# Kernel tuning notes

Measured on AMD Instinct MI355X. Metric: run time of the kernel, lower is better.

Reference implementation:

```python
import jax, jax.numpy as jnp
import numpy as np

D_MODEL = 512
D_FFN = 4 * D_MODEL
EPS = 1e-5


def layer_norm(x, gamma, beta):
    mu = jnp.mean(x, axis=-1, keepdims=True)
    var = jnp.mean(jnp.square(x - mu), axis=-1, keepdims=True)
    return (x - mu) * jax.lax.rsqrt(var + EPS) * gamma + beta


def setup_inputs() -> dict:
    key = jax.random.key(0)
    ks = jax.random.split(key, 12)
    B, S, D, F = 4, 2048, D_MODEL, D_FFN
    s = 1.0 / np.sqrt(D)
    inp = {
        "q": jax.random.normal(ks[0], (B, S, D), jnp.float32),
        "k": jax.random.normal(ks[1], (B, S, D), jnp.float32),
        "v": jax.random.normal(ks[2], (B, S, D), jnp.float32),
        "x": jax.random.normal(ks[3], (B, S, D), jnp.float32),
        "Wq": jax.random.normal(ks[4], (D, D), jnp.float32) * s,
        "bq": jnp.zeros((D,), jnp.float32),
        "Wk": jax.random.normal(ks[5], (D, D), jnp.float32) * s,
        "bk": jnp.zeros((D,), jnp.float32),
        "Wv": jax.random.normal(ks[6], (D, D), jnp.float32) * s,
        "bv": jnp.zeros((D,), jnp.float32),
        "g1": jnp.ones((D,), jnp.float32),
        "be1": jnp.zeros((D,), jnp.float32),
        "W1": jax.random.normal(ks[7], (D, F), jnp.float32) * s,
        "b1": jnp.zeros((F,), jnp.float32),
        "W2": jax.random.normal(ks[8], (F, D), jnp.float32) * (1.0 / np.sqrt(F)),
        "b2": jnp.zeros((D,), jnp.float32),
        "g2": jnp.ones((D,), jnp.float32),
        "be2": jnp.zeros((D,), jnp.float32),
    }
    return inp


def reference(q, k, v, x, Wq, bq, Wk, bk, Wv, bv, g1, be1, W1, b1, W2, b2, g2, be2):
    # QKV projections: [B,S,D] @ [D,D]
    Q = jnp.einsum("bsd,de->bse", q, Wq) + bq
    K = jnp.einsum("bsd,de->bse", k, Wk) + bk
    V = jnp.einsum("bsd,de->bse", v, Wv) + bv
    d_k = Q.shape[-1]
    # scaled dot-product attention, full [B,S,S] scores as in the original
    scores = jnp.einsum("bqd,bkd->bqk", Q, K) / jnp.sqrt(jnp.float32(d_k))
    probs = jax.nn.softmax(scores, axis=-1)
    attn = jnp.einsum("bqk,bkd->bqd", probs, V)
    # residual + LayerNorm
    h = layer_norm(attn + x, g1, be1)
    # position-wise FFN
    f = jnp.maximum(jnp.einsum("bsd,df->bsf", h, W1) + b1, 0.0)
    f = jnp.einsum("bsf,fd->bsd", f, W2) + b2
    # residual + LayerNorm
    return layer_norm(f + h, g2, be2)
```

## Files before the change

### kernel.cpp

```cpp
#include <hip/hip_runtime.h>


typedef __attribute__((ext_vector_type(8))) short short8;
typedef __attribute__((ext_vector_type(4))) float f32x4;

__device__ __forceinline__ unsigned short f2bf(float f) {
    unsigned int u = __float_as_uint(f);
    unsigned int r = (u + 0x7FFFu + ((u >> 16) & 1u)) >> 16;
    return (unsigned short)r;
}

__device__ __forceinline__ void gload_lds16(const void* g, void* l) {
    __builtin_amdgcn_global_load_lds(
        (const __attribute__((address_space(1))) void*)g,
        (__attribute__((address_space(3))) void*)l, 16, 0, 0);
}

__global__ __launch_bounds__(256) void cast_f32_bf16(
    const float* __restrict__ in, unsigned short* __restrict__ out, long n4) {
    long i = (long)blockIdx.x * blockDim.x + threadIdx.x;
    if (i < n4) {
        float4 v = ((const float4*)in)[i];
        ushort4 o;
        o.x = f2bf(v.x); o.y = f2bf(v.y); o.z = f2bf(v.z); o.w = f2bf(v.w);
        ((ushort4*)out)[i] = o;
    }
}

__global__ __launch_bounds__(256) void transpose_cast_f32_bf16(
    const float* __restrict__ in, unsigned short* __restrict__ out, int R, int C) {
    __shared__ float t[32][33];
    int c0 = blockIdx.x * 32, r0 = blockIdx.y * 32;
    int x = threadIdx.x;
    for (int i = threadIdx.y; i < 32; i += 8)
        t[i][x] = in[(long)(r0 + i) * C + c0 + x];
    __syncthreads();
    for (int i = threadIdx.y; i < 32; i += 8)
        out[(long)(c0 + i) * R + r0 + x] = f2bf(t[x][i]);
}

__global__ __launch_bounds__(256) void transpose_bf16(
    const unsigned short* __restrict__ in, unsigned short* __restrict__ out,
    int R, int C, int inLd, long inBatch, long outBatch) {
    __shared__ unsigned short t[32][33];
    long z = blockIdx.z;
    in += z * inBatch; out += z * outBatch;
    int c0 = blockIdx.x * 32, r0 = blockIdx.y * 32;
    int x = threadIdx.x;
    for (int i = threadIdx.y; i < 32; i += 8)
        t[i][x] = in[(long)(r0 + i) * inLd + c0 + x];
    __syncthreads();
    for (int i = threadIdx.y; i < 32; i += 8)
        out[(long)(c0 + i) * R + r0 + x] = t[x][i];
}

template<int BIAS, int RELU, int OUT_BF16>
__global__ __launch_bounds__(256, 2) void gemm_nt(
    const unsigned short* __restrict__ A, const unsigned short* __restrict__ BT,
    const float* __restrict__ bias, void* __restrict__ C,
    int N, int K, int lda, int ldb, int ldc,
    long aBatch, long bBatch, long cBatch, float scale) {
    __shared__ __align__(16) unsigned short As[2][4096];
    __shared__ __align__(16) unsigned short Bs[2][4096];
    const int tid  = threadIdx.x;
    const int wave = tid >> 6;
    const int lane = tid & 63;
    const long z = blockIdx.z;
    A  += z * aBatch;
    BT += z * bBatch;
    const int row0 = blockIdx.y * 128;
    const int col0 = blockIdx.x * 128;
    const int wr = (wave >> 1) * 64;
    const int wc = (wave & 1) * 64;

    f32x4 acc[4][4] = {};

    const unsigned short* Ag = A  + (long)(row0 + (tid >> 2)) * lda + (tid & 3) * 8;
    const unsigned short* Bg = BT + (long)(col0 + (tid >> 2)) * ldb + (tid & 3) * 8;
    const int sBase = wave * 512;

    const int lr  = lane & 15;
    const int kq8 = (lane >> 4) * 8;
    const int nk = K >> 5;

    #pragma unroll
    for (int c = 0; c < 2; ++c) {
        gload_lds16(Ag + (long)c * 64 * lda, &As[0][sBase + c * 2048]);
        gload_lds16(Bg + (long)c * 64 * ldb, &Bs[0][sBase + c * 2048]);
    }
    __syncthreads();

    for (int t = 0; t < nk; ++t) {
        const int cur = t & 1;
        if (t + 1 < nk) {
            const int k0 = (t + 1) << 5;
            #pragma unroll
            for (int c = 0; c < 2; ++c) {
                gload_lds16(Ag + (long)c * 64 * lda + k0, &As[cur ^ 1][sBase + c * 2048]);
                gload_lds16(Bg + (long)c * 64 * ldb + k0, &Bs[cur ^ 1][sBase + c * 2048]);
            }
        }
        short8 af[4], bf[4];
        #pragma unroll
        for (int m = 0; m < 4; ++m)
            af[m] = *(const short8*)&As[cur][(wr + m * 16 + lr) * 32 + kq8];
        #pragma unroll
        for (int n = 0; n < 4; ++n)
            bf[n] = *(const short8*)&Bs[cur][(wc + n * 16 + lr) * 32 + kq8];
        #pragma unroll
        for (int m = 0; m < 4; ++m)
            #pragma unroll
            for (int n = 0; n < 4; ++n)
                acc[m][n] = __builtin_amdgcn_mfma_f32_16x16x32_bf16(
                    af[m], bf[n], acc[m][n], 0, 0, 0);
        __syncthreads();
    }

    const int orow = row0 + wr + (lane >> 4) * 4;
    const int ocol = col0 + wc + lr;
    const long cb = z * cBatch;
    #pragma unroll
    for (int n = 0; n < 4; ++n) {
        const int cc = ocol + n * 16;
        float bv = 0.0f;
        if (BIAS) bv = bias[cc];
        #pragma unroll
        for (int m = 0; m < 4; ++m) {
            #pragma unroll
            for (int j = 0; j < 4; ++j) {
                float v = acc[m][n][j] * scale + bv;
                if (RELU) v = fmaxf(v, 0.0f);
                long off = cb + (long)(orow + m * 16 + j) * ldc + cc;
                if (OUT_BF16) ((unsigned short*)C)[off] = f2bf(v);
                else          ((float*)C)[off] = v;
            }
        }
    }
}

__global__ __launch_bounds__(256) void softmax_rows(
    const float* __restrict__ S, unsigned short* __restrict__ P) {
    long row = blockIdx.x;
    const float4* src = (const float4*)(S + row * 2048);
    int tid = threadIdx.x;
    int wave = tid >> 6, lane = tid & 63;
    float4 a = src[tid], b = src[tid + 256];
    float e[8] = { a.x, a.y, a.z, a.w, b.x, b.y, b.z, b.w };
    float m = e[0];
    #pragma unroll
    for (int i = 1; i < 8; ++i) m = fmaxf(m, e[i]);
    #pragma unroll
    for (int o = 32; o > 0; o >>= 1) m = fmaxf(m, __shfl_xor(m, o));
    __shared__ float redm[4], reds[4];
    if (lane == 0) redm[wave] = m;
    __syncthreads();
    m = fmaxf(fmaxf(redm[0], redm[1]), fmaxf(redm[2], redm[3]));
    float s = 0.0f;
    #pragma unroll
    for (int i = 0; i < 8; ++i) { e[i] = __expf(e[i] - m); s += e[i]; }
    #pragma unroll
    for (int o = 32; o > 0; o >>= 1) s += __shfl_xor(s, o);
    if (lane == 0) reds[wave] = s;
    __syncthreads();
    s = reds[0] + reds[1] + reds[2] + reds[3];
    float inv = 1.0f / s;
    ushort4 o0, o1;
    o0.x = f2bf(e[0] * inv); o0.y = f2bf(e[1] * inv);
    o0.z = f2bf(e[2] * inv); o0.w = f2bf(e[3] * inv);
    o1.x = f2bf(e[4] * inv); o1.y = f2bf(e[5] * inv);
    o1.z = f2bf(e[6] * inv); o1.w = f2bf(e[7] * inv);
    ushort4* dst = (ushort4*)(P + row * 2048);
    dst[tid] = o0;
    dst[tid + 256] = o1;
}

template<int DUAL>
__global__ __launch_bounds__(128) void ln_kernel(
    const float* __restrict__ A, const float* __restrict__ R,
    const float* __restrict__ g, const float* __restrict__ be,
    float* __restrict__ out, unsigned short* __restrict__ outbf) {
    long row = blockIdx.x;
    int tid = threadIdx.x;
    int wave = tid >> 6, lane = tid & 63;
    float4 va = ((const float4*)(A + row * 512))[tid];
    float4 vr = ((const float4*)(R + row * 512))[tid];
    float4 v;
    v.x = va.x + vr.x; v.y = va.y + vr.y; v.z = va.z + vr.z; v.w = va.w + vr.w;
    float s  = v.x + v.y + v.z + v.w;
    float s2 = v.x * v.x + v.y * v.y + v.z * v.z + v.w * v.w;
    #pragma unroll
    for (int o = 32; o > 0; o >>= 1) { s += __shfl_xor(s, o); s2 += __shfl_xor(s2, o); }
    __shared__ float r1[2], r2[2];
    if (lane == 0) { r1[wave] = s; r2[wave] = s2; }
    __syncthreads();
    s = r1[0] + r1[1]; s2 = r2[0] + r2[1];
    float mu = s * (1.0f / 512.0f);
    float var = s2 * (1.0f / 512.0f) - mu * mu;
    float rs = rsqrtf(var + 1e-5f);
    float4 gg = ((const float4*)g)[tid];
    float4 bb = ((const float4*)be)[tid];
    float4 y;
    y.x = (v.x - mu) * rs * gg.x + bb.x;
    y.y = (v.y - mu) * rs * gg.y + bb.y;
    y.z = (v.z - mu) * rs * gg.z + bb.z;
    y.w = (v.w - mu) * rs * gg.w + bb.w;
    ((float4*)(out + row * 512))[tid] = y;
    if (DUAL) {
        ushort4 o;
        o.x = f2bf(y.x); o.y = f2bf(y.y); o.z = f2bf(y.z); o.w = f2bf(y.w);
        ((ushort4*)(outbf + row * 512))[tid] = o;
    }
}

extern "C" void kernel_launch(void* const* d_in, const int* in_sizes, int n_in,
                              void* d_out, int out_size, void* d_ws, size_t ws_size,
                              hipStream_t stream) {
    const float* q   = (const float*)d_in[0];
    const float* k   = (const float*)d_in[1];
    const float* v   = (const float*)d_in[2];
    const float* x   = (const float*)d_in[3];
    const float* Wq  = (const float*)d_in[4];
    const float* bq  = (const float*)d_in[5];
    const float* Wk  = (const float*)d_in[6];
    const float* bk  = (const float*)d_in[7];
    const float* Wv  = (const float*)d_in[8];
    const float* bv  = (const float*)d_in[9];
    const float* g1  = (const float*)d_in[10];
    const float* be1 = (const float*)d_in[11];
    const float* W1  = (const float*)d_in[12];
    const float* b1  = (const float*)d_in[13];
    const float* W2  = (const float*)d_in[14];
    const float* b2  = (const float*)d_in[15];
    const float* g2  = (const float*)d_in[16];
    const float* be2 = (const float*)d_in[17];
    float* out = (float*)d_out;

    const int B = 4, S = 2048, D = 512, F = 2048;
    const long BS = (long)B * S;
    const long SD = (long)S * D;
    const long SS = (long)S * S;

    char* ws = (char*)d_ws;
    size_t off = 0;
    auto alloc = [&](size_t bytes) -> void* {
        void* p = ws + off;
        off += (bytes + 255) & ~(size_t)255;
        return p;
    };
    unsigned short* WqT = (unsigned short*)alloc((size_t)D * D * 2);
    unsigned short* WkT = (unsigned short*)alloc((size_t)D * D * 2);
    unsigned short* WvT = (unsigned short*)alloc((size_t)D * D * 2);
    unsigned short* W1T = (unsigned short*)alloc((size_t)D * F * 2);
    unsigned short* W2T = (unsigned short*)alloc((size_t)F * D * 2);
    unsigned short* qb = (unsigned short*)alloc(BS * D * 2);
    unsigned short* kb = (unsigned short*)alloc(BS * D * 2);
    unsigned short* vb = (unsigned short*)alloc(BS * D * 2);
    float* attn = (float*)qb;
    unsigned short* Qb = (unsigned short*)alloc(BS * D * 2);
    unsigned short* Kb = (unsigned short*)alloc(BS * D * 2);
    unsigned short* Vb = (unsigned short*)alloc(BS * D * 2);
    float* h_f32 = (float*)Qb;
    unsigned short* h_bf = Vb;
    unsigned short* VT = (unsigned short*)alloc(BS * D * 2);
    float* Sc = (float*)alloc((size_t)B * SS * 4);
    unsigned short* f_bf = (unsigned short*)Sc;
    float* f2 = (float*)((char*)Sc + (size_t)BS * F * 2);
    unsigned short* Pb = (unsigned short*)alloc((size_t)B * SS * 2);

    const float scale = 0.04419417382415922f;

    {
        long n4 = BS * D / 4;
        int blocks = (int)((n4 + 255) / 256);
        cast_f32_bf16<<<blocks, 256, 0, stream>>>(q, qb, n4);
        cast_f32_bf16<<<blocks, 256, 0, stream>>>(k, kb, n4);
        cast_f32_bf16<<<blocks, 256, 0, stream>>>(v, vb, n4);
    }
    transpose_cast_f32_bf16<<<dim3(D/32, D/32), dim3(32, 8), 0, stream>>>(Wq, WqT, D, D);
    transpose_cast_f32_bf16<<<dim3(D/32, D/32), dim3(32, 8), 0, stream>>>(Wk, WkT, D, D);
    transpose_cast_f32_bf16<<<dim3(D/32, D/32), dim3(32, 8), 0, stream>>>(Wv, WvT, D, D);
    transpose_cast_f32_bf16<<<dim3(F/32, D/32), dim3(32, 8), 0, stream>>>(W1, W1T, D, F);
    transpose_cast_f32_bf16<<<dim3(D/32, F/32), dim3(32, 8), 0, stream>>>(W2, W2T, F, D);
    gemm_nt<1,0,1><<<dim3(D/128, BS/128, 1), 256, 0, stream>>>(qb, WqT, bq, Qb, D, D, D, D, D, 0, 0, 0, 1.0f);
    gemm_nt<1,0,1><<<dim3(D/128, BS/128, 1), 256, 0, stream>>>(kb, WkT, bk, Kb, D, D, D, D, D, 0, 0, 0, 1.0f);
    gemm_nt<1,0,1><<<dim3(D/128, BS/128, 1), 256, 0, stream>>>(vb, WvT, bv, Vb, D, D, D, D, D, 0, 0, 0, 1.0f);
    transpose_bf16<<<dim3(D/32, S/32, B), dim3(32, 8), 0, stream>>>(Vb, VT, S, D, D, SD, SD);
    gemm_nt<0,0,0><<<dim3(S/128, S/128, B), 256, 0, stream>>>(Qb, Kb, nullptr, Sc, S, D, D, D, S, SD, SD, SS, scale);
    softmax_rows<<<(int)BS, 256, 0, stream>>>(Sc, Pb);
    gemm_nt<0,0,0><<<dim3(D/128, S/128, B), 256, 0, stream>>>(Pb, VT, nullptr, attn, D, S, S, S, D, SS, SD, SD, 1.0f);
    ln_kernel<1><<<(int)BS, 128, 0, stream>>>(attn, x, g1, be1, h_f32, h_bf);
    gemm_nt<1,1,1><<<dim3(F/128, BS/128, 1), 256, 0, stream>>>(h_bf, W1T, b1, f_bf, F, D, D, D, F, 0, 0, 0, 1.0f);
    gemm_nt<1,0,0><<<dim3(D/128, BS/128, 1), 256, 0, stream>>>(f_bf, W2T, b2, f2, D, F, F, F, D, 0, 0, 0, 1.0f);
    ln_kernel<0><<<(int)BS, 128, 0, stream>>>(f2, h_f32, g2, be2, out, nullptr);
}
```

Measured before the change: 386.1 us.

## Fuse QKV GEMMs, swizzle LDS tiles, split-K small-N GEMMs with LN reduction

Concatenates the Q/K/V weights and biases so a single GEMM launch computes all three projections, with the A operand selected per column group. Adds an XOR swizzle to the LDS tile layout to reduce bank conflicts on the MFMA fragment loads. Splits K in two for the PV and W2 GEMMs to double the block count on these low-occupancy grids. The partial sums are combined inside the LayerNorm kernels, which also absorb the b2 bias. In exchange it adds an extra fp32 partial buffer pass and a small concat kernel.

New measurement: 354.7 us. 8.1% less time.

```diff
diff --git a/kernel.cpp b/kernel.cpp
--- a/kernel.cpp
+++ b/kernel.cpp
@@ -25,6 +25,15 @@
         o.x = f2bf(v.x); o.y = f2bf(v.y); o.z = f2bf(v.z); o.w = f2bf(v.w);
         ((ushort4*)out)[i] = o;
     }
+}
+
+__global__ __launch_bounds__(256) void concat3(
+    const float* __restrict__ a, const float* __restrict__ b,
+    const float* __restrict__ c, float* __restrict__ o, int n) {
+    int i = blockIdx.x * blockDim.x + threadIdx.x;
+    if (i < n) o[i] = a[i];
+    else if (i < 2 * n) o[i] = b[i - n];
+    else if (i < 3 * n) o[i] = c[i - 2 * n];
 }
 
 __global__ __launch_bounds__(256) void transpose_cast_f32_bf16(
@@ -58,29 +67,36 @@
 __global__ __launch_bounds__(256, 2) void gemm_nt(
     const unsigned short* __restrict__ A, const unsigned short* __restrict__ BT,
     const float* __restrict__ bias, void* __restrict__ C,
-    int N, int K, int lda, int ldb, int ldc,
-    long aBatch, long bBatch, long cBatch, float scale) {
+    int K, int lda, int ldb, int ldc,
+    long aBatch, long bBatch, long cBatch,
+    long aKOff, long bKOff, long cKOff, int zDiv,
+    long aGroup, float scale) {
     __shared__ __align__(16) unsigned short As[2][4096];
     __shared__ __align__(16) unsigned short Bs[2][4096];
     const int tid  = threadIdx.x;
     const int wave = tid >> 6;
     const int lane = tid & 63;
-    const long z = blockIdx.z;
-    A  += z * aBatch;
-    BT += z * bBatch;
+    const int z = blockIdx.z;
+    const int b = z / zDiv;
+    const int kc = z - b * zDiv;
     const int row0 = blockIdx.y * 128;
     const int col0 = blockIdx.x * 128;
+    A  += (long)b * aBatch + (long)kc * aKOff + (long)(col0 >> 9) * aGroup;
+    BT += (long)b * bBatch + (long)kc * bKOff;
+    const long cOff = (long)b * cBatch + (long)kc * cKOff;
     const int wr = (wave >> 1) * 64;
     const int wc = (wave & 1) * 64;
 
     f32x4 acc[4][4] = {};
 
-    const unsigned short* Ag = A  + (long)(row0 + (tid >> 2)) * lda + (tid & 3) * 8;
-    const unsigned short* Bg = BT + (long)(col0 + (tid >> 2)) * ldb + (tid & 3) * 8;
+    const int fs = ((tid >> 2) & 3) ^ ((tid >> 4) & 3);
+    const unsigned short* Ag = A  + (long)(row0 + (tid >> 2)) * lda + (((tid & 3) ^ fs) << 3);
+    const unsigned short* Bg = BT + (long)(col0 + (tid >> 2)) * ldb + (((tid & 3) ^ fs) << 3);
     const int sBase = wave * 512;
 
     const int lr  = lane & 15;
-    const int kq8 = (lane >> 4) * 8;
+    const int fr  = (lr & 3) ^ ((lr >> 2) & 3);
+    const int kq8 = (((lane >> 4) ^ fr) << 3);
     const int nk = K >> 5;
 
     #pragma unroll
@@ -118,7 +134,6 @@
 
     const int orow = row0 + wr + (lane >> 4) * 4;
     const int ocol = col0 + wc + lr;
-    const long cb = z * cBatch;
     #pragma unroll
     for (int n = 0; n < 4; ++n) {
         const int cc = ocol + n * 16;
@@ -130,7 +145,7 @@
             for (int j = 0; j < 4; ++j) {
                 float v = acc[m][n][j] * scale + bv;
                 if (RELU) v = fmaxf(v, 0.0f);
-                long off = cb + (long)(orow + m * 16 + j) * ldc + cc;
+                long off = cOff + (long)(orow + m * 16 + j) * ldc + cc;
                 if (OUT_BF16) ((unsigned short*)C)[off] = f2bf(v);
                 else          ((float*)C)[off] = v;
             }
@@ -174,18 +189,27 @@
     dst[tid + 256] = o1;
 }
 
-template<int DUAL>
+template<int NPART, int BIASF, int DUAL>
 __global__ __launch_bounds__(128) void ln_kernel(
-    const float* __restrict__ A, const float* __restrict__ R,
+    const float* __restrict__ A0, long partOff, const float* __restrict__ R,
+    const float* __restrict__ bias,
     const float* __restrict__ g, const float* __restrict__ be,
     float* __restrict__ out, unsigned short* __restrict__ outbf) {
     long row = blockIdx.x;
     int tid = threadIdx.x;
     int wave = tid >> 6, lane = tid & 63;
-    float4 va = ((const float4*)(A + row * 512))[tid];
+    float4 va = ((const float4*)(A0 + row * 512))[tid];
     float4 vr = ((const float4*)(R + row * 512))[tid];
     float4 v;
     v.x = va.x + vr.x; v.y = va.y + vr.y; v.z = va.z + vr.z; v.w = va.w + vr.w;
+    if (NPART == 2) {
+        float4 vp = ((const float4*)(A0 + partOff + row * 512))[tid];
+        v.x += vp.x; v.y += vp.y; v.z += vp.z; v.w += vp.w;
+    }
+    if (BIASF) {
+        float4 vb = ((const float4*)bias)[tid];
+        v.x += vb.x; v.y += vb.y; v.z += vb.z; v.w += vb.w;
+    }
     float s  = v.x + v.y + v.z + v.w;
     float s2 = v.x * v.x + v.y * v.y + v.z * v.z + v.w * v.w;
     #pragma unroll
@@ -239,6 +263,7 @@
     const long BS = (long)B * S;
     const long SD = (long)S * D;
     const long SS = (long)S * S;
+    const int N3 = 3 * D;
 
     char* ws = (char*)d_ws;
     size_t off = 0;
@@ -247,49 +272,54 @@
         off += (bytes + 255) & ~(size_t)255;
         return p;
     };
-    unsigned short* WqT = (unsigned short*)alloc((size_t)D * D * 2);
-    unsigned short* WkT = (unsigned short*)alloc((size_t)D * D * 2);
-    unsigned short* WvT = (unsigned short*)alloc((size_t)D * D * 2);
-    unsigned short* W1T = (unsigned short*)alloc((size_t)D * F * 2);
-    unsigned short* W2T = (unsigned short*)alloc((size_t)F * D * 2);
-    unsigned short* qb = (unsigned short*)alloc(BS * D * 2);
-    unsigned short* kb = (unsigned short*)alloc(BS * D * 2);
-    unsigned short* vb = (unsigned short*)alloc(BS * D * 2);
-    float* attn = (float*)qb;
-    unsigned short* Qb = (unsigned short*)alloc(BS * D * 2);
-    unsigned short* Kb = (unsigned short*)alloc(BS * D * 2);
-    unsigned short* Vb = (unsigned short*)alloc(BS * D * 2);
-    float* h_f32 = (float*)Qb;
-    unsigned short* h_bf = Vb;
-    unsigned short* VT = (unsigned short*)alloc(BS * D * 2);
+    unsigned short* WqkvT = (unsigned short*)alloc((size_t)N3 * D * 2);
+    unsigned short* W1T   = (unsigned short*)alloc((size_t)D * F * 2);
+    unsigned short* W2T   = (unsigned short*)alloc((size_t)F * D * 2);
+    float* bqkv           = (float*)alloc((size_t)N3 * 4);
+    unsigned short* qkv_in = (unsigned short*)alloc(3 * BS * D * 2);
+    unsigned short* VT = qkv_in;
+    unsigned short* QKV = (unsigned short*)alloc(BS * (size_t)N3 * 2);
+    float* h_f32 = (float*)QKV;
+    unsigned short* h_bf = (unsigned short*)((char*)QKV + BS * D * 4);
     float* Sc = (float*)alloc((size_t)B * SS * 4);
-    unsigned short* f_bf = (unsigned short*)Sc;
-    float* f2 = (float*)((char*)Sc + (size_t)BS * F * 2);
+    float* attnP = Sc;
+    float* f2P   = Sc;
     unsigned short* Pb = (unsigned short*)alloc((size_t)B * SS * 2);
+    unsigned short* f_bf = Pb;
 
     const float scale = 0.04419417382415922f;
 
     {
         long n4 = BS * D / 4;
         int blocks = (int)((n4 + 255) / 256);
-        cast_f32_bf16<<<blocks, 256, 0, stream>>>(q, qb, n4);
-        cast_f32_bf16<<<blocks, 256, 0, stream>>>(k, kb, n4);
-        cast_f32_bf16<<<blocks, 256, 0, stream>>>(v, vb, n4);
-    }
-    transpose_cast_f32_bf16<<<dim3(D/32, D/32), dim3(32, 8), 0, stream>>>(Wq, WqT, D, D);
-    transpose_cast_f32_bf16<<<dim3(D/32, D/32), dim3(32, 8), 0, stream>>>(Wk, WkT, D, D);
-    transpose_cast_f32_bf16<<<dim3(D/32, D/32), dim3(32, 8), 0, stream>>>(Wv, WvT, D, D);
+        cast_f32_bf16<<<blocks, 256, 0, stream>>>(q, qkv_in, n4);
+        cast_f32_bf16<<<blocks, 256, 0, stream>>>(k, qkv_in + BS * D, n4);
+        cast_f32_bf16<<<blocks, 256, 0, stream>>>(v, qkv_in + 2 * BS * D, n4);
+    }
+    transpose_cast_f32_bf16<<<dim3(D/32, D/32), dim3(32, 8), 0, stream>>>(Wq, WqkvT, D, D);
+    transpose_cast_f32_bf16<<<dim3(D/32, D/32), dim3(32, 8), 0, stream>>>(Wk, WqkvT + (size_t)D * D, D, D);
+    transpose_cast_f32_bf16<<<dim3(D/32, D/32), dim3(32, 8), 0, stream>>>(Wv, WqkvT + 2 * (size_t)D * D, D, D);
     transpose_cast_f32_bf16<<<dim3(F/32, D/32), dim3(32, 8), 0, stream>>>(W1, W1T, D, F);
     transpose_cast_f32_bf16<<<dim3(D/32, F/32), dim3(32, 8), 0, stream>>>(W2, W2T, F, D);
-    gemm_nt<1,0,1><<<dim3(D/128, BS/128, 1), 256, 0, stream>>>(qb, WqT, bq, Qb, D, D, D, D, D, 0, 0, 0, 1.0f);
-    gemm_nt<1,0,1><<<dim3(D/128, BS/128, 1), 256, 0, stream>>>(kb, WkT, bk, Kb, D, D, D, D, D, 0, 0, 0, 1.0f);
-    gemm_nt<1,0,1><<<dim3(D/128, BS/128, 1), 256, 0, stream>>>(vb, WvT, bv, Vb, D, D, D, D, D, 0, 0, 0, 1.0f);
-    transpose_bf16<<<dim3(D/32, S/32, B), dim3(32, 8), 0, stream>>>(Vb, VT, S, D, D, SD, SD);
-    gemm_nt<0,0,0><<<dim3(S/128, S/128, B), 256, 0, stream>>>(Qb, Kb, nullptr, Sc, S, D, D, D, S, SD, SD, SS, scale);
+    concat3<<<(3 * D + 255) / 256, 256, 0, stream>>>(bq, bk, bv, bqkv, D);
+    gemm_nt<1,0,1><<<dim3(N3/128, BS/128, 1), 256, 0, stream>>>(
+        qkv_in, WqkvT, bqkv, QKV, D, D, D, N3,
+        0, 0, 0, 0, 0, 0, 1, BS * D, 1.0f);
+    transpose_bf16<<<dim3(D/32, S/32, B), dim3(32, 8), 0, stream>>>(
+        QKV + 2 * D, VT, S, D, N3, (long)S * N3, SD);
+    gemm_nt<0,0,0><<<dim3(S/128, S/128, B), 256, 0, stream>>>(
+        QKV, QKV + D, nullptr, Sc, D, N3, N3, S,
+        (long)S * N3, (long)S * N3, SS, 0, 0, 0, 1, 0, scale);
     softmax_rows<<<(int)BS, 256, 0, stream>>>(Sc, Pb);
-    gemm_nt<0,0,0><<<dim3(D/128, S/128, B), 256, 0, stream>>>(Pb, VT, nullptr, attn, D, S, S, S, D, SS, SD, SD, 1.0f);
-    ln_kernel<1><<<(int)BS, 128, 0, stream>>>(attn, x, g1, be1, h_f32, h_bf);
-    gemm_nt<1,1,1><<<dim3(F/128, BS/128, 1), 256, 0, stream>>>(h_bf, W1T, b1, f_bf, F, D, D, D, F, 0, 0, 0, 1.0f);
-    gemm_nt<1,0,0><<<dim3(D/128, BS/128, 1), 256, 0, stream>>>(f_bf, W2T, b2, f2, D, F, F, F, D, 0, 0, 0, 1.0f);
-    ln_kernel<0><<<(int)BS, 128, 0, stream>>>(f2, h_f32, g2, be2, out, nullptr);
-}
+    gemm_nt<0,0,0><<<dim3(D/128, S/128, 2 * B), 256, 0, stream>>>(
+        Pb, VT, nullptr, attnP, S / 2, S, S, D,
+        SS, SD, SD, S / 2, S / 2, BS * D, 2, 0, 1.0f);
+    ln_kernel<2,0,1><<<(int)BS, 128, 0, stream>>>(attnP, BS * D, x, nullptr, g1, be1, h_f32, h_bf);
+    gemm_nt<1,1,1><<<dim3(F/128, BS/128, 1), 256, 0, stream>>>(
+        h_bf, W1T, b1, f_bf, D, D, D, F,
+        0, 0, 0, 0, 0, 0, 1, 0, 1.0f);
+    gemm_nt<0,0,0><<<dim3(D/128, BS/128, 2), 256, 0, stream>>>(
+        f_bf, W2T, nullptr, f2P, F / 2, F, F, D,
+        0, 0, 0, F / 2, F / 2, BS * D, 2, 0, 1.0f);
+    ln_kernel<2,1,0><<<(int)BS, 128, 0, stream>>>(f2P, BS * D, h_f32, b2, g2, be2, out, nullptr);
+}
```
